# Optimization experiments

Hardware: AMD Instinct MI355X
Metric: run time of the kernel (lower is better)

## Reference

```python
import jax, jax.numpy as jnp
import numpy as np
import math

D = 768
H = 12
HD = D // H  # 64
B, N = 16, 1024
EPS = 1e-5


def _rope(x, cos, sin):
    # x: [B,N,H,hd]; cos,sin: [1,N,1,hd]
    x1, x2 = x[..., ::2], x[..., 1::2]
    return jnp.concatenate(
        [x1 * cos[..., ::2] - x2 * sin[..., ::2],
         x1 * sin[..., 1::2] + x2 * cos[..., 1::2]], axis=-1)


def setup_inputs() -> dict:
    key = jax.random.key(0)
    ks = jax.random.split(key, 8)
    s = 1.0 / math.sqrt(D)  # xavier-ish scale
    return {
        "x": jax.random.normal(ks[0], (B, N, D), jnp.float32),
        "rope_emb": jax.random.normal(ks[1], (N, HD), jnp.float32),
        "ln_w": jnp.ones((D,), jnp.float32),
        "ln_b": jnp.zeros((D,), jnp.float32),
        "enc_w": jax.random.normal(ks[2], (D, D), jnp.float32) * s,
        "enc_b": jnp.zeros((D,), jnp.float32),
        "qk_w": jax.random.normal(ks[3], (D, D), jnp.float32) * s,
        "qk_b": jnp.zeros((D,), jnp.float32),
        "v_w": jax.random.normal(ks[4], (D, D), jnp.float32) * s,
        "v_b": jnp.zeros((D,), jnp.float32),
        "out_w": jax.random.normal(ks[5], (D, D), jnp.float32) * s,
        "out_b": jnp.zeros((D,), jnp.float32),
        "gate_w": jax.random.normal(ks[6], (D, D), jnp.float32) * s,
        "gate_b": jnp.zeros((D,), jnp.float32),
    }


def reference(x, rope_emb, ln_w, ln_b, enc_w, enc_b, qk_w, qk_b,
              v_w, v_b, out_w, out_b, gate_w, gate_b):
    b, n, d = x.shape
    # Pre-LayerNorm
    mu = jnp.mean(x, axis=-1, keepdims=True)
    var = jnp.mean(jnp.square(x - mu), axis=-1, keepdims=True)
    x_norm = (x - mu) / jnp.sqrt(var + EPS) * ln_w + ln_b
    # sparse latent encoder
    x_latent = jax.nn.relu(x_norm @ enc_w.T + enc_b)
    qk = (x_latent @ qk_w.T + qk_b).reshape(b, n, H, HD)
    v = (x_latent @ v_w.T + v_b).reshape(b, n, H, HD)
    ang = rope_emb[:, :HD]
    cos = jnp.cos(ang)[None, :, None, :]
    sin = jnp.sin(ang)[None, :, None, :]
    qk = _rope(qk, cos, sin)
    # raw (softmax-free) attention, Q=K
    scores = jnp.einsum('bnhd,bmhd->bhnm', qk, qk) / math.sqrt(HD)
    attn = jnp.einsum('bhnm,bmhd->bnhd', scores, v).reshape(b, n, d)
    attn = attn @ out_w.T + out_b
    gate = jax.nn.sigmoid(x_norm @ gate_w.T + gate_b)
    return x + gate * attn
```

## Files before the change

### kernel.cpp

```cpp
#include <hip/hip_runtime.h>

typedef __bf16 bf16;
typedef __bf16 bf16x4 __attribute__((ext_vector_type(4)));
typedef __bf16 bf16x8 __attribute__((ext_vector_type(8)));
typedef float floatx4 __attribute__((ext_vector_type(4)));

#define DD 768
#define NH 12
#define HDIM 64
#define BB 16
#define NN 1024
#define MTOT (BB*NN)
#define WELEM (DD*DD)

#define ABUF 16384
#define BBUF 8192
#define TBUF (ABUF + BBUF)

__device__ __forceinline__ void async_cp16(const void* g, void* l) {
  __builtin_amdgcn_global_load_lds((const __attribute__((address_space(1))) void*)g,
                                   (__attribute__((address_space(3))) void*)l, 16, 0, 0);
}

__global__ __launch_bounds__(256) void ln_kernel(const float* __restrict__ x,
    const float* __restrict__ w, const float* __restrict__ b, bf16* __restrict__ A) {
  int row = blockIdx.x * 4 + (threadIdx.x >> 6);
  int lane = threadIdx.x & 63;
  const float4* xr = (const float4*)(x + (size_t)row * DD);
  float4 v[3];
  float s = 0.f;
#pragma unroll
  for (int i = 0; i < 3; i++) {
    v[i] = xr[lane + 64 * i];
    s += v[i].x + v[i].y + v[i].z + v[i].w;
  }
#pragma unroll
  for (int o = 32; o; o >>= 1) s += __shfl_xor(s, o);
  float mu = s * (1.f / 768.f);
  float vs = 0.f;
#pragma unroll
  for (int i = 0; i < 3; i++) {
    float dx;
    dx = v[i].x - mu; vs += dx * dx;
    dx = v[i].y - mu; vs += dx * dx;
    dx = v[i].z - mu; vs += dx * dx;
    dx = v[i].w - mu; vs += dx * dx;
  }
#pragma unroll
  for (int o = 32; o; o >>= 1) vs += __shfl_xor(vs, o);
  float rstd = rsqrtf(vs * (1.f / 768.f) + 1e-5f);
  const float4* wv = (const float4*)w;
  const float4* bv = (const float4*)b;
  bf16* Ar = A + (size_t)row * DD;
#pragma unroll
  for (int i = 0; i < 3; i++) {
    int c4 = lane + 64 * i;
    float4 ww = wv[c4], bb = bv[c4];
    bf16x4 pk;
    pk[0] = (bf16)((v[i].x - mu) * rstd * ww.x + bb.x);
    pk[1] = (bf16)((v[i].y - mu) * rstd * ww.y + bb.y);
    pk[2] = (bf16)((v[i].z - mu) * rstd * ww.z + bb.z);
    pk[3] = (bf16)((v[i].w - mu) * rstd * ww.w + bb.w);
    *(bf16x4*)(Ar + c4 * 4) = pk;
  }
}

__global__ __launch_bounds__(256) void convw_kernel(const float* __restrict__ w0,
    const float* __restrict__ w1, const float* __restrict__ w2,
    const float* __restrict__ w3, const float* __restrict__ w4, bf16* __restrict__ out) {
  int i = blockIdx.x * 256 + threadIdx.x;
  int which = i / (WELEM / 4);
  int off = (i % (WELEM / 4)) * 4;
  const float* s = which == 0 ? w0 : which == 1 ? w1 : which == 2 ? w2 : which == 3 ? w3 : w4;
  float4 v = *(const float4*)(s + off);
  bf16x4 pk;
  pk[0] = (bf16)v.x; pk[1] = (bf16)v.y; pk[2] = (bf16)v.z; pk[3] = (bf16)v.w;
  *(bf16x4*)(out + (size_t)i * 4) = pk;
}

template<int EPI>
__device__ __forceinline__ void gemm_body(
    int bm, int bn, int bnl,
    const bf16* __restrict__ Aop, const bf16* __restrict__ W,
    const float* __restrict__ bias,
    bf16* __restrict__ Cb, float* __restrict__ Cf,
    const float* __restrict__ Xres, const bf16* __restrict__ Gate,
    bf16* smem) {
  int tid = threadIdx.x;
  int w = tid >> 6, lane = tid & 63;
  int quad = lane >> 4, l16 = lane & 15;
  int wm = w >> 1, wn = w & 1;
  int sr = lane >> 3;
  int scg = (lane & 7) ^ sr;
  int swz = l16 & 7;

  const bf16* Ag = Aop + (size_t)(bm * 256) * DD;
  const bf16* Bg = W + (size_t)(bn * 128) * DD;
  const bf16* srcA = Ag + (size_t)(w * 8 + sr) * DD + scg * 8;
  const bf16* srcB = Bg + (size_t)(w * 8 + sr) * DD + scg * 8;

  floatx4 acc[4][4];
#pragma unroll
  for (int i = 0; i < 4; i++)
#pragma unroll
    for (int j = 0; j < 4; j++)
      acc[i][j] = (floatx4){0.f, 0.f, 0.f, 0.f};

  auto stageH0 = [&](int k0, bf16* buf) {
    async_cp16(srcA + (size_t)0 * (64 * DD) + k0, buf + (w + 0) * 512);
    async_cp16(srcA + (size_t)1 * (64 * DD) + k0, buf + (w + 8) * 512);
    async_cp16(srcB + k0, buf + ABUF + w * 512);
  };
  auto stageH1 = [&](int k0, bf16* buf) {
    async_cp16(srcA + (size_t)2 * (64 * DD) + k0, buf + (w + 16) * 512);
    async_cp16(srcA + (size_t)3 * (64 * DD) + k0, buf + (w + 24) * 512);
    async_cp16(srcB + (size_t)64 * DD + k0, buf + ABUF + (w + 8) * 512);
  };

  stageH0(0, smem);               stageH1(0, smem);
  stageH0(64, smem + TBUF);       stageH1(64, smem + TBUF);

#pragma unroll
  for (int t = 0; t < 12; t++) {
    if (t < 11) asm volatile("s_waitcnt vmcnt(6)" ::: "memory");
    else        asm volatile("s_waitcnt vmcnt(0)" ::: "memory");
    __builtin_amdgcn_s_barrier();
    __builtin_amdgcn_sched_barrier(0);

    const bf16* Ab = smem + (t % 3) * TBUF;
    const bf16* Bb = Ab + ABUF;
#pragma unroll
    for (int ks = 0; ks < 2; ks++) {
      int cg = (ks * 4 + quad) ^ swz;
      bf16x8 a[4], b[4];
#pragma unroll
      for (int i = 0; i < 4; i++) a[i] = *(const bf16x8*)&Ab[(wm * 64 + i * 16 + l16) * 64 + cg * 8];
#pragma unroll
      for (int i = 0; i < 4; i++) b[i] = *(const bf16x8*)&Bb[(wn * 64 + i * 16 + l16) * 64 + cg * 8];
      if (t < 10) {
        if (ks == 0) stageH0((t + 2) * 64, smem + ((t + 2) % 3) * TBUF);
        else         stageH1((t + 2) * 64, smem + ((t + 2) % 3) * TBUF);
      }
      __builtin_amdgcn_s_barrier();
      __builtin_amdgcn_sched_barrier(0);
      asm volatile("s_waitcnt lgkmcnt(0)" ::: "memory");
      __builtin_amdgcn_sched_barrier(0);
      __builtin_amdgcn_s_setprio(1);
      if (EPI == 2) {
#pragma unroll
        for (int mi = 0; mi < 4; mi++)
#pragma unroll
          for (int ni = 0; ni < 4; ni++)
            acc[mi][ni] = __builtin_amdgcn_mfma_f32_16x16x32_bf16(a[mi], b[ni], acc[mi][ni], 0, 0, 0);
      } else {
#pragma unroll
        for (int mi = 0; mi < 4; mi++)
#pragma unroll
          for (int ni = 0; ni < 4; ni++)
            acc[mi][ni] = __builtin_amdgcn_mfma_f32_16x16x32_bf16(b[ni], a[mi], acc[mi][ni], 0, 0, 0);
      }
      __builtin_amdgcn_s_setprio(0);
    }
  }

  if (EPI == 2) {
#pragma unroll
    for (int ni = 0; ni < 4; ni++) {
      int gc = bnl * 128 + wn * 64 + ni * 16 + l16;
      float bz = bias[gc];
      int h = gc >> 6, dd2 = gc & 63;
#pragma unroll
      for (int mi = 0; mi < 4; mi++) {
        int gm0 = bm * 256 + wm * 64 + mi * 16 + quad * 4;
        int b_ = gm0 >> 10, n0 = gm0 & 1023;
        bf16x4 pk;
#pragma unroll
        for (int r = 0; r < 4; r++) pk[r] = (bf16)(acc[mi][ni][r] + bz);
        *(bf16x4*)&Cb[(((size_t)b_ * NH + h) * HDIM + dd2) * NN + n0] = pk;
      }
    }
  } else {
#pragma unroll
    for (int mi = 0; mi < 4; mi++) {
      int gm = bm * 256 + wm * 64 + mi * 16 + l16;
#pragma unroll
      for (int ni = 0; ni < 4; ni++) {
        int gc = bnl * 128 + wn * 64 + ni * 16 + quad * 4;
        float4 bz = *(const float4*)&bias[gc];
        float v0 = acc[mi][ni][0] + bz.x;
        float v1 = acc[mi][ni][1] + bz.y;
        float v2 = acc[mi][ni][2] + bz.z;
        float v3 = acc[mi][ni][3] + bz.w;
        size_t idx = (size_t)gm * DD + gc;
        if (EPI == 4) {
          bf16x4 g = *(const bf16x4*)&Gate[idx];
          float4 xr = *(const float4*)&Xres[idx];
          float4 o;
          o.x = xr.x + (float)g[0] * v0;
          o.y = xr.y + (float)g[1] * v1;
          o.z = xr.z + (float)g[2] * v2;
          o.w = xr.w + (float)g[3] * v3;
          *(float4*)&Cf[idx] = o;
        } else {
          bf16x4 pk;
          if (EPI == 0) {
            pk[0] = (bf16)fmaxf(v0, 0.f); pk[1] = (bf16)fmaxf(v1, 0.f);
            pk[2] = (bf16)fmaxf(v2, 0.f); pk[3] = (bf16)fmaxf(v3, 0.f);
          } else if (EPI == 1) {
            pk[0] = (bf16)v0; pk[1] = (bf16)v1; pk[2] = (bf16)v2; pk[3] = (bf16)v3;
          } else {
            pk[0] = (bf16)(1.f / (1.f + __expf(-v0)));
            pk[1] = (bf16)(1.f / (1.f + __expf(-v1)));
            pk[2] = (bf16)(1.f / (1.f + __expf(-v2)));
            pk[3] = (bf16)(1.f / (1.f + __expf(-v3)));
          }
          *(bf16x4*)&Cb[idx] = pk;
        }
      }
    }
  }
}

template<int EPI_LO, int EPI_HI, int NBN>
__global__ __launch_bounds__(512, 2) void gemm_kernel(
    const bf16* __restrict__ Aop, const bf16* __restrict__ W,
    const float* __restrict__ bias_lo, const float* __restrict__ bias_hi,
    bf16* __restrict__ C_lo, bf16* __restrict__ C_hi, float* __restrict__ Cf,
    const float* __restrict__ Xres, const bf16* __restrict__ Gate) {
  __shared__ __attribute__((aligned(16))) bf16 smem[3 * TBUF];
  int blk = blockIdx.x;
  int xcd = blk & 7, slot = blk >> 3;
  int bm = xcd * 8 + slot / NBN;
  int bn = slot % NBN;
  if (NBN == 12 && bn >= 6) {
    gemm_body<EPI_HI>(bm, bn, bn - 6, Aop, W, bias_hi, C_hi, Cf, Xres, Gate, smem);
  } else {
    gemm_body<EPI_LO>(bm, bn, bn, Aop, W, bias_lo, C_lo, Cf, Xres, Gate, smem);
  }
}

template<int EPI>
__device__ __forceinline__ void gemm0_body(
    int bm, int bn, int bnl,
    const bf16* __restrict__ Aop, const bf16* __restrict__ W,
    const float* __restrict__ bias,
    bf16* __restrict__ Cb, float* __restrict__ Cf,
    const float* __restrict__ Xres, const bf16* __restrict__ Gate,
    bf16* As, bf16* Bs) {
  int tid = threadIdx.x;
  int wave = tid >> 6, lane = tid & 63;
  int quad = lane >> 4, l16 = lane & 15;
  int wm = wave & 1, wn = wave >> 1;
  int sr = lane >> 3;
  int smcg = (lane & 7) ^ sr;

  const bf16* Ag = Aop + (size_t)(bm * 256) * DD;
  const bf16* Bg = W + (size_t)(bn * 128) * DD;

  floatx4 acc[8][4];
#pragma unroll
  for (int i = 0; i < 8; i++)
#pragma unroll
    for (int j = 0; j < 4; j++)
      acc[i][j] = (floatx4){0.f, 0.f, 0.f, 0.f};

  int swzA = (l16 & 7);

  for (int k0 = 0; k0 < DD; k0 += 64) {
    __syncthreads();
#pragma unroll
    for (int it = 0; it < 8; it++) {
      int c = it * 4 + wave;
      int row = c * 8 + sr;
      async_cp16(Ag + (size_t)row * DD + k0 + smcg * 8, &As[c * 512]);
    }
#pragma unroll
    for (int it = 0; it < 4; it++) {
      int c = it * 4 + wave;
      int row = c * 8 + sr;
      async_cp16(Bg + (size_t)row * DD + k0 + smcg * 8, &Bs[c * 512]);
    }
    __syncthreads();
#pragma unroll
    for (int ks = 0; ks < 2; ks++) {
      int cg = (ks * 4 + quad) ^ swzA;
      bf16x8 a[8], b[4];
#pragma unroll
      for (int i = 0; i < 8; i++) a[i] = *(const bf16x8*)&As[(wm * 128 + i * 16 + l16) * 64 + cg * 8];
#pragma unroll
      for (int i = 0; i < 4; i++) b[i] = *(const bf16x8*)&Bs[(wn * 64 + i * 16 + l16) * 64 + cg * 8];
#pragma unroll
      for (int mi = 0; mi < 8; mi++)
#pragma unroll
        for (int ni = 0; ni < 4; ni++)
          acc[mi][ni] = __builtin_amdgcn_mfma_f32_16x16x32_bf16(b[ni], a[mi], acc[mi][ni], 0, 0, 0);
    }
  }

#pragma unroll
  for (int mi = 0; mi < 8; mi++) {
    int gm = bm * 256 + wm * 128 + mi * 16 + l16;
#pragma unroll
    for (int ni = 0; ni < 4; ni++) {
      int gc = bnl * 128 + wn * 64 + ni * 16 + quad * 4;
      float4 bz = *(const float4*)&bias[gc];
      float v0 = acc[mi][ni][0] + bz.x;
      float v1 = acc[mi][ni][1] + bz.y;
      float v2 = acc[mi][ni][2] + bz.z;
      float v3 = acc[mi][ni][3] + bz.w;
      size_t idx = (size_t)gm * DD + gc;
      if (EPI == 4) {
        bf16x4 g = *(const bf16x4*)&Gate[idx];
        float4 xr = *(const float4*)&Xres[idx];
        float4 o;
        o.x = xr.x + (float)g[0] * v0;
        o.y = xr.y + (float)g[1] * v1;
        o.z = xr.z + (float)g[2] * v2;
        o.w = xr.w + (float)g[3] * v3;
        *(float4*)&Cf[idx] = o;
      } else {
        bf16x4 pk;
        pk[0] = (bf16)v0; pk[1] = (bf16)v1; pk[2] = (bf16)v2; pk[3] = (bf16)v3;
        *(bf16x4*)&Cb[idx] = pk;
      }
    }
  }
}

template<int EPI, int NBN>
__global__ __launch_bounds__(256, 2) void gemm0_kernel(
    const bf16* __restrict__ Aop, const bf16* __restrict__ W,
    const float* __restrict__ bias,
    bf16* __restrict__ Cb, float* __restrict__ Cf,
    const float* __restrict__ Xres, const bf16* __restrict__ Gate) {
  __shared__ bf16 As[256 * 64];
  __shared__ bf16 Bs[128 * 64];
  int blk = blockIdx.x;
  int xcd = blk & 7, slot = blk >> 3;
  int bm = xcd * 8 + slot / NBN;
  int bn = slot % NBN;
  gemm0_body<EPI>(bm, bn, bn, Aop, W, bias, Cb, Cf, Xres, Gate, As, Bs);
}

#define TLS_S 132
__global__ __launch_bounds__(256) void rope_kernel(const bf16* __restrict__ QKraw,
    const float* __restrict__ rope, bf16* __restrict__ QKr, bf16* __restrict__ QKrT) {
  __shared__ bf16 Tls[64 * TLS_S];
  int blk = blockIdx.x;
  int bh = blk >> 3, nc = blk & 7;
  int b_ = bh / NH, h_ = bh % NH;
  int nbase = nc * 128;
  int t = threadIdx.x;
  {
    int n_loc = t >> 1, ch = t & 1;
    int n = nbase + n_loc;
    const bf16* src = QKraw + ((size_t)(b_ * NN + n)) * DD + h_ * HDIM + ch * 32;
    const float* rp = rope + n * HDIM + ch * 32;
    __attribute__((aligned(16))) bf16 o1[16];
    __attribute__((aligned(16))) bf16 o2[16];
#pragma unroll
    for (int i0 = 0; i0 < 4; i0++) {
      bf16x8 v = *(const bf16x8*)(src + i0 * 8);
      float4 r0 = *(const float4*)(rp + i0 * 8);
      float4 r1 = *(const float4*)(rp + i0 * 8 + 4);
      float a0s[4] = {r0.x, r0.z, r1.x, r1.z};
      float a1s[4] = {r0.y, r0.w, r1.y, r1.w};
#pragma unroll
      for (int p = 0; p < 4; p++) {
        float x1 = (float)v[2 * p], x2 = (float)v[2 * p + 1];
        float s0, c0, s1, c1;
        __sincosf(a0s[p], &s0, &c0);
        __sincosf(a1s[p], &s1, &c1);
        int d = i0 * 4 + p;
        o1[d] = (bf16)(x1 * c0 - x2 * s0);
        o2[d] = (bf16)(x1 * s1 + x2 * c1);
      }
    }
    bf16* dst = QKr + ((size_t)(b_ * NN + n)) * DD + h_ * HDIM;
    *(bf16x8*)&dst[ch * 16]      = *(bf16x8*)&o1[0];
    *(bf16x8*)&dst[ch * 16 + 8]  = *(bf16x8*)&o1[8];
    *(bf16x8*)&dst[32 + ch * 16]     = *(bf16x8*)&o2[0];
    *(bf16x8*)&dst[32 + ch * 16 + 8] = *(bf16x8*)&o2[8];
#pragma unroll
    for (int d = 0; d < 16; d++) {
      Tls[(ch * 16 + d) * TLS_S + n_loc] = o1[d];
      Tls[(32 + ch * 16 + d) * TLS_S + n_loc] = o2[d];
    }
  }
  __syncthreads();
  {
    int c = t >> 2, qn = t & 3;
    __attribute__((aligned(16))) bf16 buf[32];
#pragma unroll
    for (int j = 0; j < 8; j++)
      *(bf16x4*)&buf[j * 4] = *(const bf16x4*)&Tls[c * TLS_S + qn * 32 + j * 4];
    bf16* dst = QKrT + ((size_t)bh * HDIM + c) * NN + nbase + qn * 32;
#pragma unroll
    for (int j = 0; j < 4; j++)
      *(bf16x8*)&dst[j * 8] = *(bf16x8*)&buf[j * 8];
  }
}

__global__ __launch_bounds__(256) void attn_kernel(const bf16* __restrict__ QKr,
    const bf16* __restrict__ QKrT, const bf16* __restrict__ VT, bf16* __restrict__ attn) {
  __shared__ float Tp[64][64];
  __shared__ bf16 Tbf[64][72];
  int blk = blockIdx.x;
  int xcd = blk & 7, bhl = blk >> 3;
  int bh = xcd * 24 + bhl;
  int tid = threadIdx.x, wave = tid >> 6, lane = tid & 63;
  int quad = lane >> 4, l16 = lane & 15;
  const bf16* Qt = QKrT + (size_t)bh * (HDIM * NN);
  const bf16* Vt = VT + (size_t)bh * (HDIM * NN);

  floatx4 acc[4][4];
#pragma unroll
  for (int i = 0; i < 4; i++)
#pragma unroll
    for (int j = 0; j < 4; j++)
      acc[i][j] = (floatx4){0.f, 0.f, 0.f, 0.f};

  int kbase = wave * 256;
#pragma unroll
  for (int k0 = 0; k0 < 256; k0 += 32) {
    bf16x8 a[4], b[4];
#pragma unroll
    for (int i = 0; i < 4; i++) a[i] = *(const bf16x8*)&Qt[(size_t)(i * 16 + l16) * NN + kbase + k0 + quad * 8];
#pragma unroll
    for (int i = 0; i < 4; i++) b[i] = *(const bf16x8*)&Vt[(size_t)(i * 16 + l16) * NN + kbase + k0 + quad * 8];
#pragma unroll
    for (int mi = 0; mi < 4; mi++)
#pragma unroll
      for (int ni = 0; ni < 4; ni++)
        acc[mi][ni] = __builtin_amdgcn_mfma_f32_16x16x32_bf16(a[mi], b[ni], acc[mi][ni], 0, 0, 0);
  }
#pragma unroll
  for (int w = 0; w < 4; w++) {
    if (wave == w) {
#pragma unroll
      for (int mi = 0; mi < 4; mi++)
#pragma unroll
        for (int ni = 0; ni < 4; ni++)
#pragma unroll
          for (int r = 0; r < 4; r++) {
            float val = acc[mi][ni][r];
            float* p = &Tp[mi * 16 + quad * 4 + r][ni * 16 + l16];
            if (w == 0) *p = val; else *p += val;
          }
    }
    __syncthreads();
  }
  for (int e = tid; e < 4096; e += 256) {
    int d1 = e >> 6, d2 = e & 63;
    Tbf[d2][d1] = (bf16)(Tp[d1][d2] * 0.125f);
  }
  __syncthreads();

  int b_ = bh / NH, h_ = bh % NH;
  const bf16* Q = QKr + (size_t)(b_ * NN) * DD + h_ * HDIM;
  bf16* Ao = attn + (size_t)(b_ * NN) * DD + h_ * HDIM;
  bf16x8 Bf[4][2];
#pragma unroll
  for (int ni = 0; ni < 4; ni++)
#pragma unroll
    for (int ks = 0; ks < 2; ks++)
      Bf[ni][ks] = *(const bf16x8*)&Tbf[ni * 16 + l16][ks * 32 + quad * 8];

#pragma unroll
  for (int mi = 0; mi < 16; mi++) {
    int nrow = wave * 256 + mi * 16;
    bf16x8 a0 = *(const bf16x8*)&Q[(size_t)(nrow + l16) * DD + quad * 8];
    bf16x8 a1 = *(const bf16x8*)&Q[(size_t)(nrow + l16) * DD + 32 + quad * 8];
    floatx4 o[4];
#pragma unroll
    for (int ni = 0; ni < 4; ni++) o[ni] = (floatx4){0.f, 0.f, 0.f, 0.f};
#pragma unroll
    for (int ni = 0; ni < 4; ni++) {
      o[ni] = __builtin_amdgcn_mfma_f32_16x16x32_bf16(a0, Bf[ni][0], o[ni], 0, 0, 0);
      o[ni] = __builtin_amdgcn_mfma_f32_16x16x32_bf16(a1, Bf[ni][1], o[ni], 0, 0, 0);
    }
#pragma unroll
    for (int ni = 0; ni < 4; ni++)
#pragma unroll
      for (int r = 0; r < 4; r++)
        Ao[(size_t)(nrow + quad * 4 + r) * DD + ni * 16 + l16] = (bf16)o[ni][r];
  }
}

extern "C" void kernel_launch(void* const* d_in, const int* in_sizes, int n_in,
                              void* d_out, int out_size, void* d_ws, size_t ws_size,
                              hipStream_t stream) {
  const float* x      = (const float*)d_in[0];
  const float* rope   = (const float*)d_in[1];
  const float* ln_w   = (const float*)d_in[2];
  const float* ln_b   = (const float*)d_in[3];
  const float* enc_w  = (const float*)d_in[4];
  const float* enc_b  = (const float*)d_in[5];
  const float* qk_w   = (const float*)d_in[6];
  const float* qk_b   = (const float*)d_in[7];
  const float* v_w    = (const float*)d_in[8];
  const float* v_b    = (const float*)d_in[9];
  const float* out_w  = (const float*)d_in[10];
  const float* out_b  = (const float*)d_in[11];
  const float* gate_w = (const float*)d_in[12];
  const float* gate_b = (const float*)d_in[13];

  char* w = (char*)d_ws;
  const size_t S = (size_t)MTOT * DD * 2;
  bf16* s0 = (bf16*)(w);
  bf16* s1 = (bf16*)(w + S);
  bf16* s2 = (bf16*)(w + 2 * S);
  bf16* s3 = (bf16*)(w + 3 * S);
  bf16* s4 = (bf16*)(w + 4 * S);
  bf16* s5 = (bf16*)(w + 5 * S);
  bf16* Wb = (bf16*)(w + 6 * S);

  bf16* A = s0;
  bf16* L = s1;
  bf16* Gate = s2;
  bf16* QKraw = s0;
  bf16* QKr = s3;
  bf16* QKrT = s4;
  bf16* VT = s5;
  bf16* attnb = s1;

  ln_kernel<<<dim3(MTOT / 4), dim3(256), 0, stream>>>(x, ln_w, ln_b, A);
  convw_kernel<<<dim3(5 * WELEM / 4 / 256), dim3(256), 0, stream>>>(enc_w, gate_w, qk_w, v_w, out_w, Wb);

  gemm_kernel<0, 3, 12><<<dim3(768), dim3(512), 0, stream>>>(
      A, Wb, enc_b, gate_b, L, Gate, nullptr, nullptr, nullptr);
  gemm_kernel<1, 2, 12><<<dim3(768), dim3(512), 0, stream>>>(
      L, Wb + 2 * (size_t)WELEM, qk_b, v_b, QKraw, VT, nullptr, nullptr, nullptr);
  rope_kernel<<<dim3(BB * NH * 8), dim3(256), 0, stream>>>(QKraw, rope, QKr, QKrT);
  attn_kernel<<<dim3(BB * NH), dim3(256), 0, stream>>>(QKr, QKrT, VT, attnb);
  gemm0_kernel<4, 6><<<dim3(384), dim3(256), 0, stream>>>(
      attnb, Wb + 4 * (size_t)WELEM, out_b, nullptr, (float*)d_out, x, Gate);
}
```

Baseline: 336.5 us.

## Retile projection GEMMs to 128x256 with 256 threads and precompute rope sincos table

Changes the fused projection GEMMs from a 256x128 tile with 8 waves and a triple-buffered async pipeline to a 128x256 tile with 4 waves, each wave computing 128x64, using simple single-buffered loads with syncthreads per K step. Adds a small kernel that precomputes cos/sin of the rope angles into a workspace table so the rope kernel reads them instead of calling sincos per element. The retile changes the per-wave register footprint and occupancy, but loses the load/compute overlap of the previous pipeline.

```diff
diff --git a/kernel.cpp b/kernel.cpp
--- a/kernel.cpp
+++ b/kernel.cpp
@@ -12,10 +12,6 @@
 #define NN 1024
 #define MTOT (BB*NN)
 #define WELEM (DD*DD)
-
-#define ABUF 16384
-#define BBUF 8192
-#define TBUF (ABUF + BBUF)
 
 __device__ __forceinline__ void async_cp16(const void* g, void* l) {
   __builtin_amdgcn_global_load_lds((const __attribute__((address_space(1))) void*)g,
@@ -78,6 +74,16 @@
   *(bf16x4*)(out + (size_t)i * 4) = pk;
 }
 
+__global__ __launch_bounds__(256) void sincos_kernel(const float* __restrict__ rope,
+    float* __restrict__ tabs) {
+  int i = blockIdx.x * 256 + threadIdx.x;
+  float a = rope[i];
+  float s, c;
+  __sincosf(a, &s, &c);
+  tabs[i] = c;
+  tabs[65536 + i] = s;
+}
+
 template<int EPI>
 __device__ __forceinline__ void gemm_body(
     int bm, int bn, int bnl,
@@ -85,93 +91,74 @@
     const float* __restrict__ bias,
     bf16* __restrict__ Cb, float* __restrict__ Cf,
     const float* __restrict__ Xres, const bf16* __restrict__ Gate,
-    bf16* smem) {
+    bf16* As, bf16* Bs) {
   int tid = threadIdx.x;
-  int w = tid >> 6, lane = tid & 63;
+  int wave = tid >> 6, lane = tid & 63;
   int quad = lane >> 4, l16 = lane & 15;
-  int wm = w >> 1, wn = w & 1;
+  int wn = wave;
   int sr = lane >> 3;
-  int scg = (lane & 7) ^ sr;
-  int swz = l16 & 7;
-
-  const bf16* Ag = Aop + (size_t)(bm * 256) * DD;
-  const bf16* Bg = W + (size_t)(bn * 128) * DD;
-  const bf16* srcA = Ag + (size_t)(w * 8 + sr) * DD + scg * 8;
-  const bf16* srcB = Bg + (size_t)(w * 8 + sr) * DD + scg * 8;
-
-  floatx4 acc[4][4];
-#pragma unroll
-  for (int i = 0; i < 4; i++)
+  int smcg = (lane & 7) ^ sr;
+
+  const bf16* Ag = Aop + (size_t)(bm * 128) * DD;
+  const bf16* Bg = W + (size_t)(bn * 256) * DD;
+
+  floatx4 acc[8][4];
+#pragma unroll
+  for (int i = 0; i < 8; i++)
 #pragma unroll
     for (int j = 0; j < 4; j++)
       acc[i][j] = (floatx4){0.f, 0.f, 0.f, 0.f};
 
-  auto stageH0 = [&](int k0, bf16* buf) {
-    async_cp16(srcA + (size_t)0 * (64 * DD) + k0, buf + (w + 0) * 512);
-    async_cp16(srcA + (size_t)1 * (64 * DD) + k0, buf + (w + 8) * 512);
-    async_cp16(srcB + k0, buf + ABUF + w * 512);
-  };
-  auto stageH1 = [&](int k0, bf16* buf) {
-    async_cp16(srcA + (size_t)2 * (64 * DD) + k0, buf + (w + 16) * 512);
-    async_cp16(srcA + (size_t)3 * (64 * DD) + k0, buf + (w + 24) * 512);
-    async_cp16(srcB + (size_t)64 * DD + k0, buf + ABUF + (w + 8) * 512);
-  };
-
-  stageH0(0, smem);               stageH1(0, smem);
-  stageH0(64, smem + TBUF);       stageH1(64, smem + TBUF);
-
-#pragma unroll
-  for (int t = 0; t < 12; t++) {
-    if (t < 11) asm volatile("s_waitcnt vmcnt(6)" ::: "memory");
-    else        asm volatile("s_waitcnt vmcnt(0)" ::: "memory");
-    __builtin_amdgcn_s_barrier();
-    __builtin_amdgcn_sched_barrier(0);
-
-    const bf16* Ab = smem + (t % 3) * TBUF;
-    const bf16* Bb = Ab + ABUF;
+  int swz = (l16 & 7);
+
+  for (int k0 = 0; k0 < DD; k0 += 64) {
+    __syncthreads();
+#pragma unroll
+    for (int it = 0; it < 4; it++) {
+      int c = it * 4 + wave;
+      int row = c * 8 + sr;
+      async_cp16(Ag + (size_t)row * DD + k0 + smcg * 8, &As[c * 512]);
+    }
+#pragma unroll
+    for (int it = 0; it < 8; it++) {
+      int c = it * 4 + wave;
+      int row = c * 8 + sr;
+      async_cp16(Bg + (size_t)row * DD + k0 + smcg * 8, &Bs[c * 512]);
+    }
+    __syncthreads();
 #pragma unroll
     for (int ks = 0; ks < 2; ks++) {
       int cg = (ks * 4 + quad) ^ swz;
-      bf16x8 a[4], b[4];
-#pragma unroll
-      for (int i = 0; i < 4; i++) a[i] = *(const bf16x8*)&Ab[(wm * 64 + i * 16 + l16) * 64 + cg * 8];
-#pragma unroll
-      for (int i = 0; i < 4; i++) b[i] = *(const bf16x8*)&Bb[(wn * 64 + i * 16 + l16) * 64 + cg * 8];
-      if (t < 10) {
-        if (ks == 0) stageH0((t + 2) * 64, smem + ((t + 2) % 3) * TBUF);
-        else         stageH1((t + 2) * 64, smem + ((t + 2) % 3) * TBUF);
-      }
-      __builtin_amdgcn_s_barrier();
-      __builtin_amdgcn_sched_barrier(0);
-      asm volatile("s_waitcnt lgkmcnt(0)" ::: "memory");
-      __builtin_amdgcn_sched_barrier(0);
-      __builtin_amdgcn_s_setprio(1);
+      bf16x8 a[8], b[4];
+#pragma unroll
+      for (int i = 0; i < 8; i++) a[i] = *(const bf16x8*)&As[(i * 16 + l16) * 64 + cg * 8];
+#pragma unroll
+      for (int i = 0; i < 4; i++) b[i] = *(const bf16x8*)&Bs[(wn * 64 + i * 16 + l16) * 64 + cg * 8];
       if (EPI == 2) {
 #pragma unroll
-        for (int mi = 0; mi < 4; mi++)
+        for (int mi = 0; mi < 8; mi++)
 #pragma unroll
           for (int ni = 0; ni < 4; ni++)
             acc[mi][ni] = __builtin_amdgcn_mfma_f32_16x16x32_bf16(a[mi], b[ni], acc[mi][ni], 0, 0, 0);
       } else {
 #pragma unroll
-        for (int mi = 0; mi < 4; mi++)
+        for (int mi = 0; mi < 8; mi++)
 #pragma unroll
           for (int ni = 0; ni < 4; ni++)
             acc[mi][ni] = __builtin_amdgcn_mfma_f32_16x16x32_bf16(b[ni], a[mi], acc[mi][ni], 0, 0, 0);
       }
-      __builtin_amdgcn_s_setprio(0);
     }
   }
 
   if (EPI == 2) {
 #pragma unroll
     for (int ni = 0; ni < 4; ni++) {
-      int gc = bnl * 128 + wn * 64 + ni * 16 + l16;
+      int gc = bnl * 256 + wn * 64 + ni * 16 + l16;
       float bz = bias[gc];
       int h = gc >> 6, dd2 = gc & 63;
 #pragma unroll
-      for (int mi = 0; mi < 4; mi++) {
-        int gm0 = bm * 256 + wm * 64 + mi * 16 + quad * 4;
+      for (int mi = 0; mi < 8; mi++) {
+        int gm0 = bm * 128 + mi * 16 + quad * 4;
         int b_ = gm0 >> 10, n0 = gm0 & 1023;
         bf16x4 pk;
 #pragma unroll
@@ -181,11 +168,11 @@
     }
   } else {
 #pragma unroll
-    for (int mi = 0; mi < 4; mi++) {
-      int gm = bm * 256 + wm * 64 + mi * 16 + l16;
+    for (int mi = 0; mi < 8; mi++) {
+      int gm = bm * 128 + mi * 16 + l16;
 #pragma unroll
       for (int ni = 0; ni < 4; ni++) {
-        int gc = bnl * 128 + wn * 64 + ni * 16 + quad * 4;
+        int gc = bnl * 256 + wn * 64 + ni * 16 + quad * 4;
         float4 bz = *(const float4*)&bias[gc];
         float v0 = acc[mi][ni][0] + bz.x;
         float v1 = acc[mi][ni][1] + bz.y;
@@ -221,21 +208,22 @@
   }
 }
 
-template<int EPI_LO, int EPI_HI, int NBN>
-__global__ __launch_bounds__(512, 2) void gemm_kernel(
+template<int EPI_LO, int EPI_HI, int NBN, int SPLIT>
+__global__ __launch_bounds__(256, 3) void gemm_kernel(
     const bf16* __restrict__ Aop, const bf16* __restrict__ W,
     const float* __restrict__ bias_lo, const float* __restrict__ bias_hi,
     bf16* __restrict__ C_lo, bf16* __restrict__ C_hi, float* __restrict__ Cf,
     const float* __restrict__ Xres, const bf16* __restrict__ Gate) {
-  __shared__ __attribute__((aligned(16))) bf16 smem[3 * TBUF];
+  __shared__ bf16 As[128 * 64];
+  __shared__ bf16 Bs[256 * 64];
   int blk = blockIdx.x;
   int xcd = blk & 7, slot = blk >> 3;
-  int bm = xcd * 8 + slot / NBN;
+  int bm = xcd * 16 + slot / NBN;
   int bn = slot % NBN;
-  if (NBN == 12 && bn >= 6) {
-    gemm_body<EPI_HI>(bm, bn, bn - 6, Aop, W, bias_hi, C_hi, Cf, Xres, Gate, smem);
+  if (bn >= SPLIT) {
+    gemm_body<EPI_HI>(bm, bn, bn - SPLIT, Aop, W, bias_hi, C_hi, Cf, Xres, Gate, As, Bs);
   } else {
-    gemm_body<EPI_LO>(bm, bn, bn, Aop, W, bias_lo, C_lo, Cf, Xres, Gate, smem);
+    gemm_body<EPI_LO>(bm, bn, bn, Aop, W, bias_lo, C_lo, Cf, Xres, Gate, As, Bs);
   }
 }
 
@@ -344,7 +332,7 @@
 
 #define TLS_S 132
 __global__ __launch_bounds__(256) void rope_kernel(const bf16* __restrict__ QKraw,
-    const float* __restrict__ rope, bf16* __restrict__ QKr, bf16* __restrict__ QKrT) {
+    const float* __restrict__ tabs, bf16* __restrict__ QKr, bf16* __restrict__ QKrT) {
   __shared__ bf16 Tls[64 * TLS_S];
   int blk = blockIdx.x;
   int bh = blk >> 3, nc = blk & 7;
@@ -355,22 +343,24 @@
     int n_loc = t >> 1, ch = t & 1;
     int n = nbase + n_loc;
     const bf16* src = QKraw + ((size_t)(b_ * NN + n)) * DD + h_ * HDIM + ch * 32;
-    const float* rp = rope + n * HDIM + ch * 32;
+    const float* cosT = tabs + n * HDIM + ch * 32;
+    const float* sinT = tabs + 65536 + n * HDIM + ch * 32;
     __attribute__((aligned(16))) bf16 o1[16];
     __attribute__((aligned(16))) bf16 o2[16];
 #pragma unroll
     for (int i0 = 0; i0 < 4; i0++) {
       bf16x8 v = *(const bf16x8*)(src + i0 * 8);
-      float4 r0 = *(const float4*)(rp + i0 * 8);
-      float4 r1 = *(const float4*)(rp + i0 * 8 + 4);
-      float a0s[4] = {r0.x, r0.z, r1.x, r1.z};
-      float a1s[4] = {r0.y, r0.w, r1.y, r1.w};
+      float4 c01 = *(const float4*)(cosT + i0 * 8);
+      float4 c23 = *(const float4*)(cosT + i0 * 8 + 4);
+      float4 s01 = *(const float4*)(sinT + i0 * 8);
+      float4 s23 = *(const float4*)(sinT + i0 * 8 + 4);
+      float cs[8] = {c01.x, c01.y, c01.z, c01.w, c23.x, c23.y, c23.z, c23.w};
+      float ss[8] = {s01.x, s01.y, s01.z, s01.w, s23.x, s23.y, s23.z, s23.w};
 #pragma unroll
       for (int p = 0; p < 4; p++) {
         float x1 = (float)v[2 * p], x2 = (float)v[2 * p + 1];
-        float s0, c0, s1, c1;
-        __sincosf(a0s[p], &s0, &c0);
-        __sincosf(a1s[p], &s1, &c1);
+        float c0 = cs[2 * p], s0 = ss[2 * p];
+        float c1 = cs[2 * p + 1], s1 = ss[2 * p + 1];
         int d = i0 * 4 + p;
         o1[d] = (bf16)(x1 * c0 - x2 * s0);
         o2[d] = (bf16)(x1 * s1 + x2 * c1);
@@ -514,6 +504,7 @@
   bf16* s4 = (bf16*)(w + 4 * S);
   bf16* s5 = (bf16*)(w + 5 * S);
   bf16* Wb = (bf16*)(w + 6 * S);
+  float* tabs = (float*)(w + 6 * S + 6 * 1024 * 1024);
 
   bf16* A = s0;
   bf16* L = s1;
@@ -526,12 +517,13 @@
 
   ln_kernel<<<dim3(MTOT / 4), dim3(256), 0, stream>>>(x, ln_w, ln_b, A);
   convw_kernel<<<dim3(5 * WELEM / 4 / 256), dim3(256), 0, stream>>>(enc_w, gate_w, qk_w, v_w, out_w, Wb);
-
-  gemm_kernel<0, 3, 12><<<dim3(768), dim3(512), 0, stream>>>(
+  sincos_kernel<<<dim3(256), dim3(256), 0, stream>>>(rope, tabs);
+
+  gemm_kernel<0, 3, 6, 3><<<dim3(768), dim3(256), 0, stream>>>(
       A, Wb, enc_b, gate_b, L, Gate, nullptr, nullptr, nullptr);
-  gemm_kernel<1, 2, 12><<<dim3(768), dim3(512), 0, stream>>>(
+  gemm_kernel<1, 2, 6, 3><<<dim3(768), dim3(256), 0, stream>>>(
       L, Wb + 2 * (size_t)WELEM, qk_b, v_b, QKraw, VT, nullptr, nullptr, nullptr);
-  rope_kernel<<<dim3(BB * NH * 8), dim3(256), 0, stream>>>(QKraw, rope, QKr, QKrT);
+  rope_kernel<<<dim3(BB * NH * 8), dim3(256), 0, stream>>>(QKraw, tabs, QKr, QKrT);
   attn_kernel<<<dim3(BB * NH), dim3(256), 0, stream>>>(QKr, QKrT, VT, attnb);
   gemm0_kernel<4, 6><<<dim3(384), dim3(256), 0, stream>>>(
       attnb, Wb + 4 * (size_t)WELEM, out_b, nullptr, (float*)d_out, x, Gate);
```

Measured after the change: 424.3 us. 1.26x slower.

## Fuse RoPE into QK GEMM epilogue and merge prep kernels with sincos table

Applied to the files above, without the earlier changes.

Removes the standalone rope kernel by applying the rotary embedding in the QK projection GEMM epilogue, which writes both the row-major and the transposed rotated outputs directly. It also merges layernorm, weight conversion and a precomputed cos/sin table into a single prep launch. This drops one kernel launch plus a full round trip of the QK activations through global memory. In exchange, the transposed output is now written as scattered 2-byte stores with a stride of NN elements, and the row-major bf16x2 stores are also narrow, so global write coalescing may suffer.

```diff
diff --git a/kernel.cpp b/kernel.cpp
--- a/kernel.cpp
+++ b/kernel.cpp
@@ -1,6 +1,7 @@
 #include <hip/hip_runtime.h>
 
 typedef __bf16 bf16;
+typedef __bf16 bf16x2 __attribute__((ext_vector_type(2)));
 typedef __bf16 bf16x4 __attribute__((ext_vector_type(4)));
 typedef __bf16 bf16x8 __attribute__((ext_vector_type(8)));
 typedef float floatx4 __attribute__((ext_vector_type(4)));
@@ -22,60 +23,72 @@
                                    (__attribute__((address_space(3))) void*)l, 16, 0, 0);
 }
 
-__global__ __launch_bounds__(256) void ln_kernel(const float* __restrict__ x,
-    const float* __restrict__ w, const float* __restrict__ b, bf16* __restrict__ A) {
-  int row = blockIdx.x * 4 + (threadIdx.x >> 6);
-  int lane = threadIdx.x & 63;
-  const float4* xr = (const float4*)(x + (size_t)row * DD);
-  float4 v[3];
-  float s = 0.f;
-#pragma unroll
-  for (int i = 0; i < 3; i++) {
-    v[i] = xr[lane + 64 * i];
-    s += v[i].x + v[i].y + v[i].z + v[i].w;
-  }
-#pragma unroll
-  for (int o = 32; o; o >>= 1) s += __shfl_xor(s, o);
-  float mu = s * (1.f / 768.f);
-  float vs = 0.f;
-#pragma unroll
-  for (int i = 0; i < 3; i++) {
-    float dx;
-    dx = v[i].x - mu; vs += dx * dx;
-    dx = v[i].y - mu; vs += dx * dx;
-    dx = v[i].z - mu; vs += dx * dx;
-    dx = v[i].w - mu; vs += dx * dx;
-  }
-#pragma unroll
-  for (int o = 32; o; o >>= 1) vs += __shfl_xor(vs, o);
-  float rstd = rsqrtf(vs * (1.f / 768.f) + 1e-5f);
-  const float4* wv = (const float4*)w;
-  const float4* bv = (const float4*)b;
-  bf16* Ar = A + (size_t)row * DD;
-#pragma unroll
-  for (int i = 0; i < 3; i++) {
-    int c4 = lane + 64 * i;
-    float4 ww = wv[c4], bb = bv[c4];
+__global__ __launch_bounds__(256) void prep_kernel(
+    const float* __restrict__ x, const float* __restrict__ lnw,
+    const float* __restrict__ lnb, bf16* __restrict__ A,
+    const float* __restrict__ w0, const float* __restrict__ w1,
+    const float* __restrict__ w2, const float* __restrict__ w3,
+    const float* __restrict__ w4, bf16* __restrict__ Wb,
+    const float* __restrict__ rope, float* __restrict__ tabs) {
+  int blk = blockIdx.x;
+  int tid = threadIdx.x;
+  if (blk < 4096) {
+    int row = blk * 4 + (tid >> 6);
+    int lane = tid & 63;
+    const float4* xr = (const float4*)(x + (size_t)row * DD);
+    float4 v[3];
+    float s = 0.f;
+#pragma unroll
+    for (int i = 0; i < 3; i++) {
+      v[i] = xr[lane + 64 * i];
+      s += v[i].x + v[i].y + v[i].z + v[i].w;
+    }
+#pragma unroll
+    for (int o = 32; o; o >>= 1) s += __shfl_xor(s, o);
+    float mu = s * (1.f / 768.f);
+    float vs = 0.f;
+#pragma unroll
+    for (int i = 0; i < 3; i++) {
+      float dx;
+      dx = v[i].x - mu; vs += dx * dx;
+      dx = v[i].y - mu; vs += dx * dx;
+      dx = v[i].z - mu; vs += dx * dx;
+      dx = v[i].w - mu; vs += dx * dx;
+    }
+#pragma unroll
+    for (int o = 32; o; o >>= 1) vs += __shfl_xor(vs, o);
+    float rstd = rsqrtf(vs * (1.f / 768.f) + 1e-5f);
+    const float4* wv = (const float4*)lnw;
+    const float4* bv = (const float4*)lnb;
+    bf16* Ar = A + (size_t)row * DD;
+#pragma unroll
+    for (int i = 0; i < 3; i++) {
+      int c4 = lane + 64 * i;
+      float4 ww = wv[c4], bb = bv[c4];
+      bf16x4 pk;
+      pk[0] = (bf16)((v[i].x - mu) * rstd * ww.x + bb.x);
+      pk[1] = (bf16)((v[i].y - mu) * rstd * ww.y + bb.y);
+      pk[2] = (bf16)((v[i].z - mu) * rstd * ww.z + bb.z);
+      pk[3] = (bf16)((v[i].w - mu) * rstd * ww.w + bb.w);
+      *(bf16x4*)(Ar + c4 * 4) = pk;
+    }
+  } else if (blk < 4096 + 2880) {
+    int i = (blk - 4096) * 256 + tid;
+    int which = i / (WELEM / 4);
+    int off = (i % (WELEM / 4)) * 4;
+    const float* s = which == 0 ? w0 : which == 1 ? w1 : which == 2 ? w2 : which == 3 ? w3 : w4;
+    float4 v = *(const float4*)(s + off);
     bf16x4 pk;
-    pk[0] = (bf16)((v[i].x - mu) * rstd * ww.x + bb.x);
-    pk[1] = (bf16)((v[i].y - mu) * rstd * ww.y + bb.y);
-    pk[2] = (bf16)((v[i].z - mu) * rstd * ww.z + bb.z);
-    pk[3] = (bf16)((v[i].w - mu) * rstd * ww.w + bb.w);
-    *(bf16x4*)(Ar + c4 * 4) = pk;
-  }
-}
-
-__global__ __launch_bounds__(256) void convw_kernel(const float* __restrict__ w0,
-    const float* __restrict__ w1, const float* __restrict__ w2,
-    const float* __restrict__ w3, const float* __restrict__ w4, bf16* __restrict__ out) {
-  int i = blockIdx.x * 256 + threadIdx.x;
-  int which = i / (WELEM / 4);
-  int off = (i % (WELEM / 4)) * 4;
-  const float* s = which == 0 ? w0 : which == 1 ? w1 : which == 2 ? w2 : which == 3 ? w3 : w4;
-  float4 v = *(const float4*)(s + off);
-  bf16x4 pk;
-  pk[0] = (bf16)v.x; pk[1] = (bf16)v.y; pk[2] = (bf16)v.z; pk[3] = (bf16)v.w;
-  *(bf16x4*)(out + (size_t)i * 4) = pk;
+    pk[0] = (bf16)v.x; pk[1] = (bf16)v.y; pk[2] = (bf16)v.z; pk[3] = (bf16)v.w;
+    *(bf16x4*)(Wb + (size_t)i * 4) = pk;
+  } else {
+    int i = (blk - 6976) * 256 + tid;
+    float a = rope[i];
+    float s, c;
+    __sincosf(a, &s, &c);
+    tabs[i] = c;
+    tabs[65536 + i] = s;
+  }
 }
 
 template<int EPI>
@@ -83,9 +96,9 @@
     int bm, int bn, int bnl,
     const bf16* __restrict__ Aop, const bf16* __restrict__ W,
     const float* __restrict__ bias,
-    bf16* __restrict__ Cb, float* __restrict__ Cf,
+    bf16* __restrict__ Cb, bf16* __restrict__ CT, float* __restrict__ Cf,
     const float* __restrict__ Xres, const bf16* __restrict__ Gate,
-    bf16* smem) {
+    const float* __restrict__ tabs, bf16* smem) {
   int tid = threadIdx.x;
   int w = tid >> 6, lane = tid & 63;
   int quad = lane >> 4, l16 = lane & 15;
@@ -177,6 +190,41 @@
 #pragma unroll
         for (int r = 0; r < 4; r++) pk[r] = (bf16)(acc[mi][ni][r] + bz);
         *(bf16x4*)&Cb[(((size_t)b_ * NH + h) * HDIM + dd2) * NN + n0] = pk;
+      }
+    }
+  } else if (EPI == 5) {
+#pragma unroll
+    for (int mi = 0; mi < 4; mi++) {
+      int gm = bm * 256 + wm * 64 + mi * 16 + l16;
+      int b_ = gm >> 10, n = gm & 1023;
+      const float* cT = tabs + (size_t)n * 64;
+      const float* sT = tabs + 65536 + (size_t)n * 64;
+#pragma unroll
+      for (int ni = 0; ni < 4; ni++) {
+        int gc = bnl * 128 + wn * 64 + ni * 16 + quad * 4;
+        float4 bz = *(const float4*)&bias[gc];
+        float v0 = acc[mi][ni][0] + bz.x;
+        float v1 = acc[mi][ni][1] + bz.y;
+        float v2 = acc[mi][ni][2] + bz.z;
+        float v3 = acc[mi][ni][3] + bz.w;
+        int h = gc >> 6, j2 = gc & 63;
+        float4 c4 = *(const float4*)&cT[j2];
+        float4 s4 = *(const float4*)&sT[j2];
+        bf16 o1a = (bf16)(v0 * c4.x - v1 * s4.x);
+        bf16 o1b = (bf16)(v2 * c4.z - v3 * s4.z);
+        bf16 o2a = (bf16)(v0 * s4.y + v1 * c4.y);
+        bf16 o2b = (bf16)(v2 * s4.w + v3 * c4.w);
+        int p0 = j2 >> 1;
+        bf16* qr = Cb + (size_t)gm * DD + h * 64;
+        bf16x2 e0; e0[0] = o1a; e0[1] = o1b;
+        bf16x2 e1; e1[0] = o2a; e1[1] = o2b;
+        *(bf16x2*)&qr[p0] = e0;
+        *(bf16x2*)&qr[32 + p0] = e1;
+        bf16* qt = CT + ((size_t)(b_ * NH + h) * HDIM) * NN + n;
+        qt[(size_t)p0 * NN] = o1a;
+        qt[(size_t)(p0 + 1) * NN] = o1b;
+        qt[(size_t)(32 + p0) * NN] = o2a;
+        qt[(size_t)(33 + p0) * NN] = o2b;
       }
     }
   } else {
@@ -225,17 +273,19 @@
 __global__ __launch_bounds__(512, 2) void gemm_kernel(
     const bf16* __restrict__ Aop, const bf16* __restrict__ W,
     const float* __restrict__ bias_lo, const float* __restrict__ bias_hi,
-    bf16* __restrict__ C_lo, bf16* __restrict__ C_hi, float* __restrict__ Cf,
-    const float* __restrict__ Xres, const bf16* __restrict__ Gate) {
+    bf16* __restrict__ C_lo, bf16* __restrict__ C_hi, bf16* __restrict__ CT,
+    float* __restrict__ Cf,
+    const float* __restrict__ Xres, const bf16* __restrict__ Gate,
+    const float* __restrict__ tabs) {
   __shared__ __attribute__((aligned(16))) bf16 smem[3 * TBUF];
   int blk = blockIdx.x;
   int xcd = blk & 7, slot = blk >> 3;
   int bm = xcd * 8 + slot / NBN;
   int bn = slot % NBN;
   if (NBN == 12 && bn >= 6) {
-    gemm_body<EPI_HI>(bm, bn, bn - 6, Aop, W, bias_hi, C_hi, Cf, Xres, Gate, smem);
+    gemm_body<EPI_HI>(bm, bn, bn - 6, Aop, W, bias_hi, C_hi, CT, Cf, Xres, Gate, tabs, smem);
   } else {
-    gemm_body<EPI_LO>(bm, bn, bn, Aop, W, bias_lo, C_lo, Cf, Xres, Gate, smem);
+    gemm_body<EPI_LO>(bm, bn, bn, Aop, W, bias_lo, C_lo, CT, Cf, Xres, Gate, tabs, smem);
   }
 }
 
@@ -342,65 +392,6 @@
   gemm0_body<EPI>(bm, bn, bn, Aop, W, bias, Cb, Cf, Xres, Gate, As, Bs);
 }
 
-#define TLS_S 132
-__global__ __launch_bounds__(256) void rope_kernel(const bf16* __restrict__ QKraw,
-    const float* __restrict__ rope, bf16* __restrict__ QKr, bf16* __restrict__ QKrT) {
-  __shared__ bf16 Tls[64 * TLS_S];
-  int blk = blockIdx.x;
-  int bh = blk >> 3, nc = blk & 7;
-  int b_ = bh / NH, h_ = bh % NH;
-  int nbase = nc * 128;
-  int t = threadIdx.x;
-  {
-    int n_loc = t >> 1, ch = t & 1;
-    int n = nbase + n_loc;
-    const bf16* src = QKraw + ((size_t)(b_ * NN + n)) * DD + h_ * HDIM + ch * 32;
-    const float* rp = rope + n * HDIM + ch * 32;
-    __attribute__((aligned(16))) bf16 o1[16];
-    __attribute__((aligned(16))) bf16 o2[16];
-#pragma unroll
-    for (int i0 = 0; i0 < 4; i0++) {
-      bf16x8 v = *(const bf16x8*)(src + i0 * 8);
-      float4 r0 = *(const float4*)(rp + i0 * 8);
-      float4 r1 = *(const float4*)(rp + i0 * 8 + 4);
-      float a0s[4] = {r0.x, r0.z, r1.x, r1.z};
-      float a1s[4] = {r0.y, r0.w, r1.y, r1.w};
-#pragma unroll
-      for (int p = 0; p < 4; p++) {
-        float x1 = (float)v[2 * p], x2 = (float)v[2 * p + 1];
-        float s0, c0, s1, c1;
-        __sincosf(a0s[p], &s0, &c0);
-        __sincosf(a1s[p], &s1, &c1);
-        int d = i0 * 4 + p;
-        o1[d] = (bf16)(x1 * c0 - x2 * s0);
-        o2[d] = (bf16)(x1 * s1 + x2 * c1);
-      }
-    }
-    bf16* dst = QKr + ((size_t)(b_ * NN + n)) * DD + h_ * HDIM;
-    *(bf16x8*)&dst[ch * 16]      = *(bf16x8*)&o1[0];
-    *(bf16x8*)&dst[ch * 16 + 8]  = *(bf16x8*)&o1[8];
-    *(bf16x8*)&dst[32 + ch * 16]     = *(bf16x8*)&o2[0];
-    *(bf16x8*)&dst[32 + ch * 16 + 8] = *(bf16x8*)&o2[8];
-#pragma unroll
-    for (int d = 0; d < 16; d++) {
-      Tls[(ch * 16 + d) * TLS_S + n_loc] = o1[d];
-      Tls[(32 + ch * 16 + d) * TLS_S + n_loc] = o2[d];
-    }
-  }
-  __syncthreads();
-  {
-    int c = t >> 2, qn = t & 3;
-    __attribute__((aligned(16))) bf16 buf[32];
-#pragma unroll
-    for (int j = 0; j < 8; j++)
-      *(bf16x4*)&buf[j * 4] = *(const bf16x4*)&Tls[c * TLS_S + qn * 32 + j * 4];
-    bf16* dst = QKrT + ((size_t)bh * HDIM + c) * NN + nbase + qn * 32;
-#pragma unroll
-    for (int j = 0; j < 4; j++)
-      *(bf16x8*)&dst[j * 8] = *(bf16x8*)&buf[j * 8];
-  }
-}
-
 __global__ __launch_bounds__(256) void attn_kernel(const bf16* __restrict__ QKr,
     const bf16* __restrict__ QKrT, const bf16* __restrict__ VT, bf16* __restrict__ attn) {
   __shared__ float Tp[64][64];
@@ -514,24 +505,23 @@
   bf16* s4 = (bf16*)(w + 4 * S);
   bf16* s5 = (bf16*)(w + 5 * S);
   bf16* Wb = (bf16*)(w + 6 * S);
+  float* tabs = (float*)(w + 6 * S + 6 * 1024 * 1024);
 
   bf16* A = s0;
   bf16* L = s1;
   bf16* Gate = s2;
-  bf16* QKraw = s0;
   bf16* QKr = s3;
   bf16* QKrT = s4;
   bf16* VT = s5;
   bf16* attnb = s1;
 
-  ln_kernel<<<dim3(MTOT / 4), dim3(256), 0, stream>>>(x, ln_w, ln_b, A);
-  convw_kernel<<<dim3(5 * WELEM / 4 / 256), dim3(256), 0, stream>>>(enc_w, gate_w, qk_w, v_w, out_w, Wb);
+  prep_kernel<<<dim3(7232), dim3(256), 0, stream>>>(
+      x, ln_w, ln_b, A, enc_w, gate_w, qk_w, v_w, out_w, Wb, rope, tabs);
 
   gemm_kernel<0, 3, 12><<<dim3(768), dim3(512), 0, stream>>>(
-      A, Wb, enc_b, gate_b, L, Gate, nullptr, nullptr, nullptr);
-  gemm_kernel<1, 2, 12><<<dim3(768), dim3(512), 0, stream>>>(
-      L, Wb + 2 * (size_t)WELEM, qk_b, v_b, QKraw, VT, nullptr, nullptr, nullptr);
-  rope_kernel<<<dim3(BB * NH * 8), dim3(256), 0, stream>>>(QKraw, rope, QKr, QKrT);
+      A, Wb, enc_b, gate_b, L, Gate, nullptr, nullptr, nullptr, nullptr, nullptr);
+  gemm_kernel<5, 2, 12><<<dim3(768), dim3(512), 0, stream>>>(
+      L, Wb + 2 * (size_t)WELEM, qk_b, v_b, QKr, VT, QKrT, nullptr, nullptr, nullptr, tabs);
   attn_kernel<<<dim3(BB * NH), dim3(256), 0, stream>>>(QKr, QKrT, VT, attnb);
   gemm0_kernel<4, 6><<<dim3(384), dim3(256), 0, stream>>>(
       attnb, Wb + 4 * (size_t)WELEM, out_b, nullptr, (float*)d_out, x, Gate);
```

Measured after the change: 328.6 us. 1.02x faster.
